# Kernel optimization log

Hardware: AMD Instinct MI355X
Metric: run time of the kernel (lower is better)

The kernel has to match this reference:

```python
import jax, jax.numpy as jnp
import numpy as np

B, S = 16, 32768
LEVELS = (5, 20)
TIME_DIM = 8
NUM_FREQS = 6  # frequency xyz encoder: 3*(1+2*6)=39 dims
HID = 128
IN_DIM = 3 * (1 + 2 * NUM_FREQS) + 2 * TIME_DIM  # 55


def setup_inputs() -> dict:
    key = jax.random.key(0)
    ks = jax.random.split(key, 16)
    time = jax.random.uniform(ks[0], (B,), dtype=jnp.float32)
    xyz = jax.random.uniform(ks[1], (B, S, 3), dtype=jnp.float32) * 2.0 - 1.0  # in [-1,1]
    te0 = jax.random.normal(ks[2], (LEVELS[0] + 1, TIME_DIM), dtype=jnp.float32)
    te1 = jax.random.normal(ks[3], (LEVELS[1] + 1, TIME_DIM), dtype=jnp.float32)
    W0 = jax.random.normal(ks[4], (IN_DIM, HID), dtype=jnp.float32) * 0.05
    b0 = jnp.zeros((HID,), dtype=jnp.float32)
    W1 = jax.random.normal(ks[5], (HID, HID), dtype=jnp.float32) * 0.05
    b1 = jnp.zeros((HID,), dtype=jnp.float32)
    W2 = jax.random.normal(ks[6], (HID, HID), dtype=jnp.float32) * 0.05
    b2 = jnp.zeros((HID,), dtype=jnp.float32)
    Wout = jax.random.normal(ks[7], (HID, 1), dtype=jnp.float32) * 0.05
    bout = jnp.zeros((1,), dtype=jnp.float32)
    return {"time": time, "xyz": xyz, "te0": te0, "te1": te1,
            "W0": W0, "b0": b0, "W1": W1, "b1": b1, "W2": W2, "b2": b2,
            "Wout": Wout, "bout": bout}


def _time_encode(t, emb, L):
    # bucketize t into L uniform intervals on [0,1), lerp between bucket endpoints
    tL = t * L
    idx = jnp.clip(jnp.floor(tL).astype(jnp.int32), 0, L - 1)  # (B,)
    w = (idx + 1).astype(t.dtype) - tL                          # weight for lower endpoint
    lerped = w[:, None] * emb[idx] + (1.0 - w)[:, None] * emb[idx + 1]
    # t >= 1: use last embedding directly (torch fallback branch)
    return jnp.where((t >= 1.0)[:, None], emb[L][None, :], lerped)


def _xyz_encode(x):
    # frequency encoding, include_input, freqs 2^0..2^(NUM_FREQS-1)
    freqs = jnp.asarray(2.0 ** np.arange(NUM_FREQS), dtype=x.dtype)  # (F,)
    xp = x[:, None, :] * freqs[None, :, None]                         # (N, F, 3)
    n = x.shape[0]
    return jnp.concatenate([x, jnp.sin(xp).reshape(n, -1), jnp.cos(xp).reshape(n, -1)], axis=-1)


def reference(time, xyz, te0, te1, W0, b0, W1, b1, W2, b2, Wout, bout):
    s = xyz.shape[1]
    t_enc = jnp.concatenate([_time_encode(time, te0, LEVELS[0]),
                             _time_encode(time, te1, LEVELS[1])], axis=-1)  # (B, 16)
    t_enc = jnp.repeat(t_enc, s, axis=0)          # (B*S, 16)  'B d -> (B S) d'
    pts = (xyz.reshape(-1, 3) + 1.0) / 2.0        # (B*S, 3)
    x = jnp.concatenate([t_enc, _xyz_encode(pts)], axis=1)  # (B*S, 55)
    x = jax.nn.relu(x @ W0 + b0)
    x = jax.nn.relu(x @ W1 + b1)
    x = jax.nn.relu(x @ W2 + b2)
    return x @ Wout + bout  # (B*S, 1)
```

## Files before the change

kernel.cpp:

```cpp
#include <hip/hip_runtime.h>

typedef _Float16 f16;
typedef __attribute__((ext_vector_type(2))) __fp16 fp16x2;
typedef __attribute__((ext_vector_type(8))) _Float16 f16x8;
typedef __attribute__((ext_vector_type(4))) float f32x4;
typedef __attribute__((ext_vector_type(4))) unsigned int u32x4;

#define NPTS   (16 * 32768)
#define W0P_OFF 0
#define W1P_OFF (16 * 1024)
#define W2P_OFF (48 * 1024)
#define WOP_OFF (80 * 1024)
#define FRAGS_BYTES (84 * 1024)
#define TENC_OFF FRAGS_BYTES
#define WS_NEEDED (FRAGS_BYTES + 1024)
#define LDS_TOTAL (8 * 4096)

__global__ void pack_weights(const float* __restrict__ time, const float* __restrict__ te0,
                             const float* __restrict__ te1, const float* __restrict__ W0,
                             const float* __restrict__ W1, const float* __restrict__ W2,
                             const float* __restrict__ Wout, unsigned char* __restrict__ ws) {
  const int bi = blockIdx.x;
  const int l = threadIdx.x;
  const int g = l >> 4, r16 = l & 15;
  if (bi < 84) {
    const float* W; int obase, fi, kt, mt, kmax; bool natural, outcol;
    if (bi < 16)      { W = W0;   fi = bi;      mt = fi >> 1; kt = fi & 1; obase = W0P_OFF; kmax = 55;  natural = true;  outcol = false; }
    else if (bi < 48) { W = W1;   fi = bi - 16; mt = fi >> 2; kt = fi & 3; obase = W1P_OFF; kmax = 128; natural = false; outcol = false; }
    else if (bi < 80) { W = W2;   fi = bi - 48; mt = fi >> 2; kt = fi & 3; obase = W2P_OFF; kmax = 128; natural = false; outcol = false; }
    else              { W = Wout; fi = bi - 80; mt = 0;       kt = fi;     obase = WOP_OFF; kmax = 128; natural = false; outcol = true;  }
    const int m = mt * 16 + r16;
    f16 vals[8] __attribute__((aligned(16)));
#pragma unroll
    for (int j = 0; j < 8; ++j) {
      const int k = natural ? (kt * 32 + g * 8 + j)
                            : (kt * 32 + (j >> 2) * 16 + g * 4 + (j & 3));
      float v = 0.f;
      if (k < kmax) v = outcol ? ((m == 0) ? Wout[k] : 0.f) : W[k * 128 + m];
      vals[j] = (f16)v;
    }
    *(u32x4*)(ws + obase + (fi * 64 + l) * 16) = *(const u32x4*)vals;
  } else {
    const int idx = (bi - 84) * 64 + l;
    const int b = idx >> 4, d = idx & 15;
    const float t = time[b];
    const float* emb; int L, dd;
    if (d < 8) { emb = te0; L = 5;  dd = d; }
    else       { emb = te1; L = 20; dd = d - 8; }
    const float tL = t * (float)L;
    int i = (int)floorf(tL);
    i = i < 0 ? 0 : (i > L - 1 ? L - 1 : i);
    const float wlo = (float)(i + 1) - tL;
    float v = wlo * emb[i * 8 + dd] + (1.f - wlo) * emb[(i + 1) * 8 + dd];
    if (t >= 1.f) v = emb[L * 8 + dd];
    ((float*)(ws + TENC_OFF))[idx] = v;
  }
}

template <int KT>
__device__ __forceinline__ void layer_swapped(const unsigned char* __restrict__ wsrc,
                                              const float* __restrict__ bias,
                                              const f16x8 (&Bin)[KT][4], f16x8 (&Bout)[4][4],
                                              int lane) {
  const int g4 = (lane >> 4) * 4;
#pragma unroll
  for (int mtp = 0; mtp < 4; ++mtp) {
    const float4 ba = *(const float4*)(bias + mtp * 32 + g4);
    const float4 bb = *(const float4*)(bias + mtp * 32 + 16 + g4);
    f32x4 acc[2][4];
#pragma unroll
    for (int nt = 0; nt < 4; ++nt) {
      acc[0][nt] = (f32x4){ba.x, ba.y, ba.z, ba.w};
      acc[1][nt] = (f32x4){bb.x, bb.y, bb.z, bb.w};
    }
    __builtin_amdgcn_s_setprio(1);
#pragma unroll
    for (int kt = 0; kt < KT; ++kt) {
      const f16x8 A0 = *(const f16x8*)(wsrc + (((2 * mtp)     * KT + kt) * 64 + lane) * 16);
      const f16x8 A1 = *(const f16x8*)(wsrc + (((2 * mtp + 1) * KT + kt) * 64 + lane) * 16);
#pragma unroll
      for (int nt = 0; nt < 4; ++nt)
        acc[0][nt] = __builtin_amdgcn_mfma_f32_16x16x32_f16(A0, Bin[kt][nt], acc[0][nt], 0, 0, 0);
#pragma unroll
      for (int nt = 0; nt < 4; ++nt)
        acc[1][nt] = __builtin_amdgcn_mfma_f32_16x16x32_f16(A1, Bin[kt][nt], acc[1][nt], 0, 0, 0);
    }
    __builtin_amdgcn_s_setprio(0);
#pragma unroll
    for (int nt = 0; nt < 4; ++nt) {
      union { fp16x2 h2[4]; f16x8 v; } u;
      u.h2[0] = __builtin_amdgcn_cvt_pkrtz(fmaxf(acc[0][nt][0], 0.f), fmaxf(acc[0][nt][1], 0.f));
      u.h2[1] = __builtin_amdgcn_cvt_pkrtz(fmaxf(acc[0][nt][2], 0.f), fmaxf(acc[0][nt][3], 0.f));
      u.h2[2] = __builtin_amdgcn_cvt_pkrtz(fmaxf(acc[1][nt][0], 0.f), fmaxf(acc[1][nt][1], 0.f));
      u.h2[3] = __builtin_amdgcn_cvt_pkrtz(fmaxf(acc[1][nt][2], 0.f), fmaxf(acc[1][nt][3], 0.f));
      Bout[mtp][nt] = u.v;
    }
  }
}

__global__ void __launch_bounds__(512, 2)
mlp_main(const float* __restrict__ xyz, const float* __restrict__ b0,
         const float* __restrict__ b1, const float* __restrict__ b2,
         const float* __restrict__ bout, const unsigned char* __restrict__ ws,
         float* __restrict__ out) {
  extern __shared__ char lds[];
  const int tid = threadIdx.x;
  const int lane = tid & 63, wv = tid >> 6;
  const int g = lane >> 4, r16 = lane & 15;

  char* scr = lds + wv * 4096;
  const float bo = bout[0];

  const int pbase = blockIdx.x * 512 + wv * 64;
  const int p = pbase + lane;

  f16 feat[64] __attribute__((aligned(16)));
  const float* tb = (const float*)(ws + TENC_OFF) + (blockIdx.x >> 6) * 16;
#pragma unroll
  for (int i = 0; i < 16; ++i) feat[i] = (f16)tb[i];
  const float xs0 = xyz[p * 3], xs1 = xyz[p * 3 + 1], xs2 = xyz[p * 3 + 2];
  const float pcs[3] = {(xs0 + 1.f) * 0.5f, (xs1 + 1.f) * 0.5f, (xs2 + 1.f) * 0.5f};
#pragma unroll
  for (int c = 0; c < 3; ++c) {
    feat[16 + c] = (f16)pcs[c];
    float s = __sinf(pcs[c]), co = __cosf(pcs[c]);
#pragma unroll
    for (int f = 0; f < 6; ++f) {
      feat[19 + f * 3 + c] = (f16)s;
      feat[37 + f * 3 + c] = (f16)co;
      const float s2 = 2.f * s * co, c2 = 1.f - 2.f * s * s;
      s = s2; co = c2;
    }
  }
#pragma unroll
  for (int i = 55; i < 64; ++i) feat[i] = (f16)0.f;

  f16x8 B0[2][4];
#pragma unroll
  for (int h = 0; h < 2; ++h) {
    if ((lane >> 5) == h) {
#pragma unroll
      for (int s = 0; s < 8; ++s)
        *(u32x4*)(scr + (lane & 31) * 128 + ((s ^ (lane & 7)) * 16)) = ((const u32x4*)feat)[s];
    }
    asm volatile("s_waitcnt lgkmcnt(0)" ::: "memory");
#pragma unroll
    for (int kt = 0; kt < 2; ++kt)
#pragma unroll
      for (int nn = 0; nn < 2; ++nn) {
        const int row = nn * 16 + r16;
        B0[kt][h * 2 + nn] = *(const f16x8*)(scr + row * 128 + (((4 * kt + g) ^ (row & 7)) * 16));
      }
    asm volatile("s_waitcnt lgkmcnt(0)" ::: "memory");
  }

  f16x8 Bx[4][4], By[4][4];
  layer_swapped<2>(ws + W0P_OFF, b0, B0, Bx, lane);
  layer_swapped<4>(ws + W1P_OFF, b1, Bx, By, lane);
  layer_swapped<4>(ws + W2P_OFF, b2, By, Bx, lane);

  f32x4 accO[4];
#pragma unroll
  for (int nt = 0; nt < 4; ++nt) accO[nt] = (f32x4){bo, bo, bo, bo};
  __builtin_amdgcn_s_setprio(1);
#pragma unroll
  for (int kt = 0; kt < 4; ++kt) {
    const f16x8 A = *(const f16x8*)(ws + WOP_OFF + (kt * 64 + lane) * 16);
#pragma unroll
    for (int nt = 0; nt < 4; ++nt)
      accO[nt] = __builtin_amdgcn_mfma_f32_16x16x32_f16(A, Bx[kt][nt], accO[nt], 0, 0, 0);
  }
  __builtin_amdgcn_s_setprio(0);

  const float a0 = __shfl(accO[0][0], r16, 64);
  const float a1 = __shfl(accO[1][0], r16, 64);
  const float a2 = __shfl(accO[2][0], r16, 64);
  const float a3 = __shfl(accO[3][0], r16, 64);
  const float v = g == 0 ? a0 : g == 1 ? a1 : g == 2 ? a2 : a3;
  out[pbase + lane] = v;
}

extern "C" void kernel_launch(void* const* d_in, const int* in_sizes, int n_in,
                              void* d_out, int out_size, void* d_ws, size_t ws_size,
                              hipStream_t stream) {
  const float* time = (const float*)d_in[0];
  const float* xyz  = (const float*)d_in[1];
  const float* te0  = (const float*)d_in[2];
  const float* te1  = (const float*)d_in[3];
  const float* W0   = (const float*)d_in[4];
  const float* b0   = (const float*)d_in[5];
  const float* W1   = (const float*)d_in[6];
  const float* b1   = (const float*)d_in[7];
  const float* W2   = (const float*)d_in[8];
  const float* b2   = (const float*)d_in[9];
  const float* Wout = (const float*)d_in[10];
  const float* bout = (const float*)d_in[11];
  float* out = (float*)d_out;
  unsigned char* ws = (unsigned char*)d_ws;
  if (ws_size < WS_NEEDED) return;

  pack_weights<<<88, 64, 0, stream>>>(time, te0, te1, W0, W1, W2, Wout, ws);
  mlp_main<<<NPTS / 512, 512, LDS_TOTAL, stream>>>(xyz, b0, b1, b2, bout, ws, out);
}
```

Measured before the change: 54.48 us.

## Software-pipeline weight fragment loads with 3-stage buffer and widen M tiles per pass

Restructures each MLP layer to compute four 16-row M tiles per pass (two passes instead of four), with weight A-fragments prefetched two k-steps ahead through a triple-buffered register array. Bias is added after the MFMA chain instead of seeding the accumulator. Launch bounds drop from 2 to 1 blocks per CU, allowing more registers per thread for the larger accumulator set at the cost of occupancy. The intent is to hide global/L2 latency of weight loads behind MFMA work and reuse each B fragment across more MFMAs.

```diff
diff --git a/kernel.cpp b/kernel.cpp
--- a/kernel.cpp
+++ b/kernel.cpp
@@ -63,42 +63,60 @@
                                               const f16x8 (&Bin)[KT][4], f16x8 (&Bout)[4][4],
                                               int lane) {
   const int g4 = (lane >> 4) * 4;
-#pragma unroll
-  for (int mtp = 0; mtp < 4; ++mtp) {
-    const float4 ba = *(const float4*)(bias + mtp * 32 + g4);
-    const float4 bb = *(const float4*)(bias + mtp * 32 + 16 + g4);
-    f32x4 acc[2][4];
-#pragma unroll
-    for (int nt = 0; nt < 4; ++nt) {
-      acc[0][nt] = (f32x4){ba.x, ba.y, ba.z, ba.w};
-      acc[1][nt] = (f32x4){bb.x, bb.y, bb.z, bb.w};
-    }
-    __builtin_amdgcn_s_setprio(1);
+  f16x8 Ab[3][4];
+#pragma unroll
+  for (int s = 0; s < 2; ++s) {
+    const int q = s / KT, kt = s % KT;
+#pragma unroll
+    for (int m = 0; m < 4; ++m)
+      Ab[s][m] = *(const f16x8*)(wsrc + (((4 * q + m) * KT + kt) * 64 + lane) * 16);
+  }
+#pragma unroll
+  for (int q = 0; q < 2; ++q) {
+    float4 bv[4];
+#pragma unroll
+    for (int i = 0; i < 4; ++i)
+      bv[i] = *(const float4*)(bias + q * 64 + i * 16 + g4);
+    f32x4 acc[4][4];
+#pragma unroll
+    for (int m = 0; m < 4; ++m)
+#pragma unroll
+      for (int nt = 0; nt < 4; ++nt) acc[m][nt] = (f32x4){0.f, 0.f, 0.f, 0.f};
 #pragma unroll
     for (int kt = 0; kt < KT; ++kt) {
-      const f16x8 A0 = *(const f16x8*)(wsrc + (((2 * mtp)     * KT + kt) * 64 + lane) * 16);
-      const f16x8 A1 = *(const f16x8*)(wsrc + (((2 * mtp + 1) * KT + kt) * 64 + lane) * 16);
-#pragma unroll
-      for (int nt = 0; nt < 4; ++nt)
-        acc[0][nt] = __builtin_amdgcn_mfma_f32_16x16x32_f16(A0, Bin[kt][nt], acc[0][nt], 0, 0, 0);
-#pragma unroll
-      for (int nt = 0; nt < 4; ++nt)
-        acc[1][nt] = __builtin_amdgcn_mfma_f32_16x16x32_f16(A1, Bin[kt][nt], acc[1][nt], 0, 0, 0);
-    }
-    __builtin_amdgcn_s_setprio(0);
-#pragma unroll
-    for (int nt = 0; nt < 4; ++nt) {
-      union { fp16x2 h2[4]; f16x8 v; } u;
-      u.h2[0] = __builtin_amdgcn_cvt_pkrtz(fmaxf(acc[0][nt][0], 0.f), fmaxf(acc[0][nt][1], 0.f));
-      u.h2[1] = __builtin_amdgcn_cvt_pkrtz(fmaxf(acc[0][nt][2], 0.f), fmaxf(acc[0][nt][3], 0.f));
-      u.h2[2] = __builtin_amdgcn_cvt_pkrtz(fmaxf(acc[1][nt][0], 0.f), fmaxf(acc[1][nt][1], 0.f));
-      u.h2[3] = __builtin_amdgcn_cvt_pkrtz(fmaxf(acc[1][nt][2], 0.f), fmaxf(acc[1][nt][3], 0.f));
-      Bout[mtp][nt] = u.v;
-    }
-  }
-}
-
-__global__ void __launch_bounds__(512, 2)
+      const int s = q * KT + kt, cb = s % 3;
+      if (s + 2 < 2 * KT) {
+        const int q2 = (s + 2) / KT, kt2 = (s + 2) % KT, pb = (s + 2) % 3;
+#pragma unroll
+        for (int m = 0; m < 4; ++m)
+          Ab[pb][m] = *(const f16x8*)(wsrc + (((4 * q2 + m) * KT + kt2) * 64 + lane) * 16);
+      }
+      __builtin_amdgcn_s_setprio(1);
+#pragma unroll
+      for (int m = 0; m < 4; ++m)
+#pragma unroll
+        for (int nt = 0; nt < 4; ++nt)
+          acc[m][nt] = __builtin_amdgcn_mfma_f32_16x16x32_f16(Ab[cb][m], Bin[kt][nt], acc[m][nt], 0, 0, 0);
+      __builtin_amdgcn_s_setprio(0);
+    }
+#pragma unroll
+    for (int h = 0; h < 2; ++h) {
+      const float* bap = (const float*)&bv[2 * h];
+      const float* bbp = (const float*)&bv[2 * h + 1];
+#pragma unroll
+      for (int nt = 0; nt < 4; ++nt) {
+        union { fp16x2 h2[4]; f16x8 v; } u;
+        u.h2[0] = __builtin_amdgcn_cvt_pkrtz(fmaxf(acc[2*h][nt][0] + bap[0], 0.f), fmaxf(acc[2*h][nt][1] + bap[1], 0.f));
+        u.h2[1] = __builtin_amdgcn_cvt_pkrtz(fmaxf(acc[2*h][nt][2] + bap[2], 0.f), fmaxf(acc[2*h][nt][3] + bap[3], 0.f));
+        u.h2[2] = __builtin_amdgcn_cvt_pkrtz(fmaxf(acc[2*h+1][nt][0] + bbp[0], 0.f), fmaxf(acc[2*h+1][nt][1] + bbp[1], 0.f));
+        u.h2[3] = __builtin_amdgcn_cvt_pkrtz(fmaxf(acc[2*h+1][nt][2] + bbp[2], 0.f), fmaxf(acc[2*h+1][nt][3] + bbp[3], 0.f));
+        Bout[2 * q + h][nt] = u.v;
+      }
+    }
+  }
+}
+
+__global__ void __launch_bounds__(512, 1)
 mlp_main(const float* __restrict__ xyz, const float* __restrict__ b0,
          const float* __restrict__ b1, const float* __restrict__ b2,
          const float* __restrict__ bout, const unsigned char* __restrict__ ws,
@@ -159,18 +177,22 @@
   layer_swapped<4>(ws + W1P_OFF, b1, Bx, By, lane);
   layer_swapped<4>(ws + W2P_OFF, b2, By, Bx, lane);
 
+  f16x8 Ab[3];
+  Ab[0] = *(const f16x8*)(ws + WOP_OFF + (0 * 64 + lane) * 16);
+  Ab[1] = *(const f16x8*)(ws + WOP_OFF + (1 * 64 + lane) * 16);
   f32x4 accO[4];
 #pragma unroll
   for (int nt = 0; nt < 4; ++nt) accO[nt] = (f32x4){bo, bo, bo, bo};
-  __builtin_amdgcn_s_setprio(1);
 #pragma unroll
   for (int kt = 0; kt < 4; ++kt) {
-    const f16x8 A = *(const f16x8*)(ws + WOP_OFF + (kt * 64 + lane) * 16);
+    if (kt + 2 < 4)
+      Ab[(kt + 2) % 3] = *(const f16x8*)(ws + WOP_OFF + ((kt + 2) * 64 + lane) * 16);
+    __builtin_amdgcn_s_setprio(1);
 #pragma unroll
     for (int nt = 0; nt < 4; ++nt)
-      accO[nt] = __builtin_amdgcn_mfma_f32_16x16x32_f16(A, Bx[kt][nt], accO[nt], 0, 0, 0);
-  }
-  __builtin_amdgcn_s_setprio(0);
+      accO[nt] = __builtin_amdgcn_mfma_f32_16x16x32_f16(Ab[kt % 3], Bx[kt][nt], accO[nt], 0, 0, 0);
+    __builtin_amdgcn_s_setprio(0);
+  }
 
   const float a0 = __shfl(accO[0][0], r16, 64);
   const float a1 = __shfl(accO[1][0], r16, 64);
```

Measured after the change: 50.76 us. -6.8%, faster.

## Switch MLP to 32x32x16 MFMA with weight fragments staged in LDS

Applied to the files above, without the earlier changes.

Replaces the 16x16x32 MFMA tiling with 32x32x16 MFMA tiles and repacks the weight fragments to match. All packed weights (88 KB) are copied into LDS once per block, so the A-operand loads in each layer read from shared memory instead of global or L2. Occupancy drops from two blocks per CU to one because of the much larger LDS footprint, and each block pays an upfront copy plus a barrier. Features are now built in fp32 and packed to fp16 pairs before the LDS transpose.

```diff
diff --git a/kernel.cpp b/kernel.cpp
--- a/kernel.cpp
+++ b/kernel.cpp
@@ -3,18 +3,19 @@
 typedef _Float16 f16;
 typedef __attribute__((ext_vector_type(2))) __fp16 fp16x2;
 typedef __attribute__((ext_vector_type(8))) _Float16 f16x8;
-typedef __attribute__((ext_vector_type(4))) float f32x4;
+typedef __attribute__((ext_vector_type(16))) float f32x16;
 typedef __attribute__((ext_vector_type(4))) unsigned int u32x4;
 
-#define NPTS   (16 * 32768)
-#define W0P_OFF 0
-#define W1P_OFF (16 * 1024)
-#define W2P_OFF (48 * 1024)
-#define WOP_OFF (80 * 1024)
-#define FRAGS_BYTES (84 * 1024)
+#define NPTS (16 * 32768)
+#define W0F 0
+#define W1F (16 * 1024)
+#define W2F (48 * 1024)
+#define WOF (80 * 1024)
+#define FRAGS_BYTES (88 * 1024)
 #define TENC_OFF FRAGS_BYTES
 #define WS_NEEDED (FRAGS_BYTES + 1024)
-#define LDS_TOTAL (8 * 4096)
+#define SCR_OFF FRAGS_BYTES
+#define LDS_TOTAL (SCR_OFF + 8 * 4096)
 
 __global__ void pack_weights(const float* __restrict__ time, const float* __restrict__ te0,
                              const float* __restrict__ te1, const float* __restrict__ W0,
@@ -22,26 +23,27 @@
                              const float* __restrict__ Wout, unsigned char* __restrict__ ws) {
   const int bi = blockIdx.x;
   const int l = threadIdx.x;
-  const int g = l >> 4, r16 = l & 15;
-  if (bi < 84) {
-    const float* W; int obase, fi, kt, mt, kmax; bool natural, outcol;
-    if (bi < 16)      { W = W0;   fi = bi;      mt = fi >> 1; kt = fi & 1; obase = W0P_OFF; kmax = 55;  natural = true;  outcol = false; }
-    else if (bi < 48) { W = W1;   fi = bi - 16; mt = fi >> 2; kt = fi & 3; obase = W1P_OFF; kmax = 128; natural = false; outcol = false; }
-    else if (bi < 80) { W = W2;   fi = bi - 48; mt = fi >> 2; kt = fi & 3; obase = W2P_OFF; kmax = 128; natural = false; outcol = false; }
-    else              { W = Wout; fi = bi - 80; mt = 0;       kt = fi;     obase = WOP_OFF; kmax = 128; natural = false; outcol = true;  }
-    const int m = mt * 16 + r16;
+  const int h = l >> 5, r32 = l & 31;
+  if (bi < 88) {
+    const float* W; int obase, mt, kt, kmax; bool natural, outcol;
+    if (bi < 16)      { W = W0;   mt = bi >> 2;        kt = bi & 3;  obase = W0F; kmax = 55;  natural = true;  outcol = false; }
+    else if (bi < 48) { W = W1;   mt = (bi - 16) >> 3; kt = (bi - 16) & 7; obase = W1F; kmax = 128; natural = false; outcol = false; }
+    else if (bi < 80) { W = W2;   mt = (bi - 48) >> 3; kt = (bi - 48) & 7; obase = W2F; kmax = 128; natural = false; outcol = false; }
+    else              { W = Wout; mt = 0;              kt = bi - 80; obase = WOF; kmax = 128; natural = false; outcol = true;  }
+    const int m = mt * 32 + r32;
+    const int fi = outcol ? kt : (bi < 16 ? mt * 4 + kt : mt * 8 + kt);
     f16 vals[8] __attribute__((aligned(16)));
 #pragma unroll
     for (int j = 0; j < 8; ++j) {
-      const int k = natural ? (kt * 32 + g * 8 + j)
-                            : (kt * 32 + (j >> 2) * 16 + g * 4 + (j & 3));
+      const int kl = natural ? (8 * h + j) : ((j & 3) + 8 * (j >> 2) + 4 * h);
+      const int k = kt * 16 + kl;
       float v = 0.f;
-      if (k < kmax) v = outcol ? ((m == 0) ? Wout[k] : 0.f) : W[k * 128 + m];
+      if (k < kmax) v = outcol ? ((r32 == 0) ? Wout[k] : 0.f) : W[k * 128 + m];
       vals[j] = (f16)v;
     }
     *(u32x4*)(ws + obase + (fi * 64 + l) * 16) = *(const u32x4*)vals;
   } else {
-    const int idx = (bi - 84) * 64 + l;
+    const int idx = (bi - 88) * 64 + l;
     const int b = idx >> 4, d = idx & 15;
     const float t = time[b];
     const float* emb; int L, dd;
@@ -58,47 +60,45 @@
 }
 
 template <int KT>
-__device__ __forceinline__ void layer_swapped(const unsigned char* __restrict__ wsrc,
-                                              const float* __restrict__ bias,
-                                              const f16x8 (&Bin)[KT][4], f16x8 (&Bout)[4][4],
-                                              int lane) {
-  const int g4 = (lane >> 4) * 4;
-#pragma unroll
-  for (int mtp = 0; mtp < 4; ++mtp) {
-    const float4 ba = *(const float4*)(bias + mtp * 32 + g4);
-    const float4 bb = *(const float4*)(bias + mtp * 32 + 16 + g4);
-    f32x4 acc[2][4];
-#pragma unroll
-    for (int nt = 0; nt < 4; ++nt) {
-      acc[0][nt] = (f32x4){ba.x, ba.y, ba.z, ba.w};
-      acc[1][nt] = (f32x4){bb.x, bb.y, bb.z, bb.w};
-    }
+__device__ __forceinline__ void layer32(const char* __restrict__ wlds,
+                                        const float* __restrict__ bias,
+                                        const f16x8 (&Bin)[2][KT], f16x8 (&Bout)[2][8],
+                                        int lane) {
+  const int h = lane >> 5;
+#pragma unroll
+  for (int mt = 0; mt < 4; ++mt) {
+    f32x16 c;
+#pragma unroll
+    for (int q = 0; q < 4; ++q) {
+      const float4 b4 = *(const float4*)(bias + mt * 32 + q * 8 + 4 * h);
+      c[4 * q] = b4.x; c[4 * q + 1] = b4.y; c[4 * q + 2] = b4.z; c[4 * q + 3] = b4.w;
+    }
+    f32x16 a0 = c, a1 = c;
     __builtin_amdgcn_s_setprio(1);
 #pragma unroll
     for (int kt = 0; kt < KT; ++kt) {
-      const f16x8 A0 = *(const f16x8*)(wsrc + (((2 * mtp)     * KT + kt) * 64 + lane) * 16);
-      const f16x8 A1 = *(const f16x8*)(wsrc + (((2 * mtp + 1) * KT + kt) * 64 + lane) * 16);
-#pragma unroll
-      for (int nt = 0; nt < 4; ++nt)
-        acc[0][nt] = __builtin_amdgcn_mfma_f32_16x16x32_f16(A0, Bin[kt][nt], acc[0][nt], 0, 0, 0);
-#pragma unroll
-      for (int nt = 0; nt < 4; ++nt)
-        acc[1][nt] = __builtin_amdgcn_mfma_f32_16x16x32_f16(A1, Bin[kt][nt], acc[1][nt], 0, 0, 0);
+      const f16x8 A = *(const f16x8*)(wlds + ((mt * KT + kt) * 64 + lane) * 16);
+      a0 = __builtin_amdgcn_mfma_f32_32x32x16_f16(A, Bin[0][kt], a0, 0, 0, 0);
+      a1 = __builtin_amdgcn_mfma_f32_32x32x16_f16(A, Bin[1][kt], a1, 0, 0, 0);
     }
     __builtin_amdgcn_s_setprio(0);
 #pragma unroll
-    for (int nt = 0; nt < 4; ++nt) {
-      union { fp16x2 h2[4]; f16x8 v; } u;
-      u.h2[0] = __builtin_amdgcn_cvt_pkrtz(fmaxf(acc[0][nt][0], 0.f), fmaxf(acc[0][nt][1], 0.f));
-      u.h2[1] = __builtin_amdgcn_cvt_pkrtz(fmaxf(acc[0][nt][2], 0.f), fmaxf(acc[0][nt][3], 0.f));
-      u.h2[2] = __builtin_amdgcn_cvt_pkrtz(fmaxf(acc[1][nt][0], 0.f), fmaxf(acc[1][nt][1], 0.f));
-      u.h2[3] = __builtin_amdgcn_cvt_pkrtz(fmaxf(acc[1][nt][2], 0.f), fmaxf(acc[1][nt][3], 0.f));
-      Bout[mtp][nt] = u.v;
-    }
-  }
-}
-
-__global__ void __launch_bounds__(512, 2)
+    for (int f = 0; f < 2; ++f) {
+      union { fp16x2 h2[4]; f16x8 v; } u0, u1;
+#pragma unroll
+      for (int pq = 0; pq < 4; ++pq) {
+        u0.h2[pq] = __builtin_amdgcn_cvt_pkrtz(fmaxf(a0[8 * f + 2 * pq], 0.f),
+                                               fmaxf(a0[8 * f + 2 * pq + 1], 0.f));
+        u1.h2[pq] = __builtin_amdgcn_cvt_pkrtz(fmaxf(a1[8 * f + 2 * pq], 0.f),
+                                               fmaxf(a1[8 * f + 2 * pq + 1], 0.f));
+      }
+      Bout[0][2 * mt + f] = u0.v;
+      Bout[1][2 * mt + f] = u1.v;
+    }
+  }
+}
+
+__global__ void __launch_bounds__(512, 1)
 mlp_main(const float* __restrict__ xyz, const float* __restrict__ b0,
          const float* __restrict__ b1, const float* __restrict__ b2,
          const float* __restrict__ bout, const unsigned char* __restrict__ ws,
@@ -106,78 +106,82 @@
   extern __shared__ char lds[];
   const int tid = threadIdx.x;
   const int lane = tid & 63, wv = tid >> 6;
-  const int g = lane >> 4, r16 = lane & 15;
-
-  char* scr = lds + wv * 4096;
+  const int h = lane >> 5, r32 = lane & 31;
+
+  for (int i = tid; i < FRAGS_BYTES / 16; i += 512)
+    *(u32x4*)(lds + i * 16) = *(const u32x4*)(ws + i * 16);
+  __syncthreads();
+
+  char* scr = lds + SCR_OFF + wv * 4096;
   const float bo = bout[0];
 
   const int pbase = blockIdx.x * 512 + wv * 64;
   const int p = pbase + lane;
 
-  f16 feat[64] __attribute__((aligned(16)));
+  float ff[64];
   const float* tb = (const float*)(ws + TENC_OFF) + (blockIdx.x >> 6) * 16;
 #pragma unroll
-  for (int i = 0; i < 16; ++i) feat[i] = (f16)tb[i];
+  for (int i = 0; i < 16; ++i) ff[i] = tb[i];
   const float xs0 = xyz[p * 3], xs1 = xyz[p * 3 + 1], xs2 = xyz[p * 3 + 2];
   const float pcs[3] = {(xs0 + 1.f) * 0.5f, (xs1 + 1.f) * 0.5f, (xs2 + 1.f) * 0.5f};
 #pragma unroll
   for (int c = 0; c < 3; ++c) {
-    feat[16 + c] = (f16)pcs[c];
+    ff[16 + c] = pcs[c];
     float s = __sinf(pcs[c]), co = __cosf(pcs[c]);
 #pragma unroll
     for (int f = 0; f < 6; ++f) {
-      feat[19 + f * 3 + c] = (f16)s;
-      feat[37 + f * 3 + c] = (f16)co;
+      ff[19 + f * 3 + c] = s;
+      ff[37 + f * 3 + c] = co;
       const float s2 = 2.f * s * co, c2 = 1.f - 2.f * s * s;
       s = s2; co = c2;
     }
   }
 #pragma unroll
-  for (int i = 55; i < 64; ++i) feat[i] = (f16)0.f;
+  for (int i = 55; i < 64; ++i) ff[i] = 0.f;
+  unsigned int fw[32];
+#pragma unroll
+  for (int i = 0; i < 32; ++i) {
+    union { fp16x2 hh; unsigned int u; } cv;
+    cv.hh = __builtin_amdgcn_cvt_pkrtz(ff[2 * i], ff[2 * i + 1]);
+    fw[i] = cv.u;
+  }
 
   f16x8 B0[2][4];
 #pragma unroll
-  for (int h = 0; h < 2; ++h) {
-    if ((lane >> 5) == h) {
+  for (int nh = 0; nh < 2; ++nh) {
+    if (h == nh) {
 #pragma unroll
       for (int s = 0; s < 8; ++s)
-        *(u32x4*)(scr + (lane & 31) * 128 + ((s ^ (lane & 7)) * 16)) = ((const u32x4*)feat)[s];
+        *(u32x4*)(scr + r32 * 128 + ((s ^ (r32 & 7)) * 16)) = ((const u32x4*)fw)[s];
     }
     asm volatile("s_waitcnt lgkmcnt(0)" ::: "memory");
 #pragma unroll
-    for (int kt = 0; kt < 2; ++kt)
-#pragma unroll
-      for (int nn = 0; nn < 2; ++nn) {
-        const int row = nn * 16 + r16;
-        B0[kt][h * 2 + nn] = *(const f16x8*)(scr + row * 128 + (((4 * kt + g) ^ (row & 7)) * 16));
-      }
+    for (int kt = 0; kt < 4; ++kt)
+      B0[nh][kt] = *(const f16x8*)(scr + r32 * 128 + (((2 * kt + h) ^ (r32 & 7)) * 16));
     asm volatile("s_waitcnt lgkmcnt(0)" ::: "memory");
   }
 
-  f16x8 Bx[4][4], By[4][4];
-  layer_swapped<2>(ws + W0P_OFF, b0, B0, Bx, lane);
-  layer_swapped<4>(ws + W1P_OFF, b1, Bx, By, lane);
-  layer_swapped<4>(ws + W2P_OFF, b2, By, Bx, lane);
-
-  f32x4 accO[4];
-#pragma unroll
-  for (int nt = 0; nt < 4; ++nt) accO[nt] = (f32x4){bo, bo, bo, bo};
+  f16x8 Bx[2][8], By[2][8];
+  layer32<4>((const char*)lds + W0F, b0, B0, Bx, lane);
+  layer32<8>((const char*)lds + W1F, b1, Bx, By, lane);
+  layer32<8>((const char*)lds + W2F, b2, By, Bx, lane);
+
+  f32x16 o0, o1;
+#pragma unroll
+  for (int r = 0; r < 16; ++r) { o0[r] = bo; o1[r] = bo; }
   __builtin_amdgcn_s_setprio(1);
 #pragma unroll
-  for (int kt = 0; kt < 4; ++kt) {
-    const f16x8 A = *(const f16x8*)(ws + WOP_OFF + (kt * 64 + lane) * 16);
-#pragma unroll
-    for (int nt = 0; nt < 4; ++nt)
-      accO[nt] = __builtin_amdgcn_mfma_f32_16x16x32_f16(A, Bx[kt][nt], accO[nt], 0, 0, 0);
+  for (int kt = 0; kt < 8; ++kt) {
+    const f16x8 A = *(const f16x8*)((const char*)lds + WOF + (kt * 64 + lane) * 16);
+    o0 = __builtin_amdgcn_mfma_f32_32x32x16_f16(A, Bx[0][kt], o0, 0, 0, 0);
+    o1 = __builtin_amdgcn_mfma_f32_32x32x16_f16(A, Bx[1][kt], o1, 0, 0, 0);
   }
   __builtin_amdgcn_s_setprio(0);
 
-  const float a0 = __shfl(accO[0][0], r16, 64);
-  const float a1 = __shfl(accO[1][0], r16, 64);
-  const float a2 = __shfl(accO[2][0], r16, 64);
-  const float a3 = __shfl(accO[3][0], r16, 64);
-  const float v = g == 0 ? a0 : g == 1 ? a1 : g == 2 ? a2 : a3;
-  out[pbase + lane] = v;
+  if (lane < 32) {
+    out[pbase + lane] = o0[0];
+    out[pbase + 32 + lane] = o1[0];
+  }
 }
 
 extern "C" void kernel_launch(void* const* d_in, const int* in_sizes, int n_in,
@@ -199,6 +203,9 @@
   unsigned char* ws = (unsigned char*)d_ws;
   if (ws_size < WS_NEEDED) return;
 
-  pack_weights<<<88, 64, 0, stream>>>(time, te0, te1, W0, W1, W2, Wout, ws);
+  hipFuncSetAttribute((const void*)mlp_main,
+                      hipFuncAttributeMaxDynamicSharedMemorySize, LDS_TOTAL);
+
+  pack_weights<<<92, 64, 0, stream>>>(time, te0, te1, W0, W1, W2, Wout, ws);
   mlp_main<<<NPTS / 512, 512, LDS_TOTAL, stream>>>(xyz, b0, b1, b2, bout, ws, out);
 }
```

Measured after the change: 56.10 us. 1.03x slower.
